# Kernel optimization log

Measured on AMD Instinct MI355X. Metric: run time of the kernel, lower is better.

The kernel has to match this reference:

```python
import jax, jax.numpy as jnp
import numpy as np

NUM_HEADS = 16
LN_EPS = 1e-5
RMS_EPS = 1e-6


def rmsnorm(x, gamma, eps=RMS_EPS):
    xf = x.astype(jnp.float32)
    rms = jax.lax.rsqrt(jnp.mean(xf * xf, axis=-1, keepdims=True) + eps)
    return gamma * (xf * rms).astype(x.dtype)


def layernorm(x, g, b, eps=LN_EPS):
    mu = jnp.mean(x, axis=-1, keepdims=True)
    var = jnp.mean(jnp.square(x - mu), axis=-1, keepdims=True)
    return (x - mu) * jax.lax.rsqrt(var + eps) * g + b


def setup_inputs() -> dict:
    key = jax.random.key(0)
    E = 2048
    ks = jax.random.split(key, 10)
    std = 0.02
    inp = {
        "x": jax.random.normal(ks[0], (2, 2048, E), dtype=jnp.float32),
        "Wq": jax.random.normal(ks[1], (E, E), dtype=jnp.float32) * std,
        "Wk": jax.random.normal(ks[2], (E, E), dtype=jnp.float32) * std,
        "Wv": jax.random.normal(ks[3], (E, E), dtype=jnp.float32) * std,
        "Wo": jax.random.normal(ks[4], (E, E), dtype=jnp.float32) * std,
        "ln_g": jnp.ones((E,), jnp.float32),
        "ln_b": jnp.zeros((E,), jnp.float32),
        "rms_g": jnp.ones((E,), jnp.float32),
        "mlp_W0": jax.random.normal(ks[5], (E, E), dtype=jnp.float32) * std,
        "sw_W": jax.random.normal(ks[6], (E, E), dtype=jnp.float32) * std,
        "sw_V": jax.random.normal(ks[7], (E, E), dtype=jnp.float32) * std,
        "sw_beta": jnp.ones((1,), jnp.float32),
        "mlp_rms_g": jnp.ones((E,), jnp.float32),
    }
    return inp


def reference(x, Wq, Wk, Wv, Wo, ln_g, ln_b, rms_g, mlp_W0, sw_W, sw_V, sw_beta, mlp_rms_g):
    B, S, E = x.shape
    H = NUM_HEADS
    Dh = E // H
    scale = 1.0 / (Dh ** 0.5)

    # --- MultiheadAttention (faithful to original einsum/view quirks) ---
    q = x @ Wq.T                     # (B,S,E)
    k = (x @ Wk.T) * scale
    v = x @ Wv.T
    qh = q.reshape(B, S, H, Dh)
    kh = k.reshape(B, S, H, Dh)
    scores = jnp.einsum('bthd,bshd->bhts', qh, kh)        # (B,H,T,S)
    causal = jnp.tril(jnp.ones((S, S), dtype=bool))
    scores = jnp.where(causal, scores, -jnp.inf)
    attn = jax.nn.softmax(scores, axis=-1)
    # NOTE: v is split (B,S,Dh,H) -- head/head_dim axes swapped vs q/k, as in the torch code
    vh = v.reshape(B, S, Dh, H)
    ctx = jnp.einsum('bsdh,bhts->bthd', vh, attn)          # == torch 'kjlm,kmij->kiml'
    ctx = ctx.reshape(B, S, E)                              # flatten heads-major
    ctx = layernorm(ctx, ln_g, ln_b)
    attn_out = ctx @ Wo.T

    x = x + attn_out
    x = rmsnorm(x, rms_g)

    # --- MLP: Linear -> SwiGLU -> RMSNorm, residual ---
    h = x @ mlp_W0.T
    w = h @ sw_W.T
    swish = w * jax.nn.sigmoid(sw_beta * w)
    g = swish * (h @ sw_V.T)
    mlp_out = rmsnorm(g, mlp_rms_g)
    return x + mlp_out
```

## Files before the change

kernel.cpp:

```cpp
#include <hip/hip_runtime.h>


#define B_    2
#define S_    2048
#define E_    2048
#define H_    16
#define DH    128
#define MROWS 4096
#define NEGF  (-3.0e38f)

typedef unsigned short ushort_t;
typedef unsigned int   uint_t;
typedef ushort_t us8   __attribute__((ext_vector_type(8)));
typedef ushort_t us4   __attribute__((ext_vector_type(4)));
typedef __bf16   bf16x8 __attribute__((ext_vector_type(8)));
typedef float    f32x4 __attribute__((ext_vector_type(4)));

__device__ __forceinline__ float b2f(ushort_t u) {
    uint_t x = ((uint_t)u) << 16;
    union { uint_t u; float f; } c; c.u = x; return c.f;
}
__device__ __forceinline__ ushort_t f2b(float f) {
    union { float f; uint_t u; } c; c.f = f;
    uint_t x = c.u;
    uint_t r = (x + 0x7fffu + ((x >> 16) & 1u)) >> 16;
    return (ushort_t)r;
}
__device__ __forceinline__ float fexp2(float x) {
    return __builtin_amdgcn_exp2f(x);
}

__device__ __forceinline__ void gld16(const ushort_t* g, ushort_t* l) {
    __builtin_amdgcn_global_load_lds(
        (const __attribute__((address_space(1))) void*)g,
        (__attribute__((address_space(3))) void*)l,
        16, 0, 0);
}

__global__ void probe_dtype(const ushort_t* w, int* flag) {
    __shared__ int cnt;
    if (threadIdx.x == 0) cnt = 0;
    __syncthreads();
    int c = 0;
    for (int i = threadIdx.x; i < 4096; i += 256) {
        uint_t e = (w[i] >> 7) & 0xFFu;
        if (e >= 0x84u) c++;
    }
    atomicAdd(&cnt, c);
    __syncthreads();
    if (threadIdx.x == 0) *flag = (cnt >= 8) ? 1 : 0;
}

__global__ void convert_k(const void* src, ushort_t* dst, long n, const int* flag) {
    int f = *flag;
    long i0 = (long)blockIdx.x * blockDim.x + threadIdx.x;
    long stride = (long)gridDim.x * blockDim.x;
    long n4 = n >> 2;
    if (f) {
        const f32x4* s = (const f32x4*)src;
        for (long i = i0; i < n4; i += stride) {
            f32x4 v = s[i];
            us4 o = { f2b(v[0]), f2b(v[1]), f2b(v[2]), f2b(v[3]) };
            *(us4*)(dst + i * 4) = o;
        }
        for (long i = n4 * 4 + i0; i < n; i += stride)
            dst[i] = f2b(((const float*)src)[i]);
    } else {
        const us4* s = (const us4*)src;
        for (long i = i0; i < n4; i += stride)
            *(us4*)(dst + i * 4) = s[i];
        for (long i = n4 * 4 + i0; i < n; i += stride)
            dst[i] = ((const ushort_t*)src)[i];
    }
}

__global__ void fill_diag(float* out, long n, float val) {
    long i = (long)blockIdx.x * 256 + threadIdx.x;
    if (i < n) out[i] = val;
}

__global__ __launch_bounds__(256) void gemm_bt(
    const ushort_t* __restrict__ A, const ushort_t* __restrict__ W,
    ushort_t* out, const ushort_t* resid, const ushort_t* beta,
    void* outv, const int* flagp, float scale, int mode)
{
    const int K = E_, N = E_;
    __shared__ alignas(16) ushort_t Asf[128 * 32];
    __shared__ alignas(16) ushort_t Bsf[128 * 32];

    const int tid  = threadIdx.x;
    const int wave = tid >> 6;
    const int lane = tid & 63;
    const int wm   = (wave >> 1) * 64;
    const int wn   = (wave & 1) * 64;
    const int lrow = lane & 15;
    const int quad = lane >> 4;
    const int m0   = blockIdx.y * 128;
    const int n0   = blockIdx.x * 128;

    const float betav = (beta != nullptr) ? b2f(beta[0]) : 0.0f;
    const int   of32  = (flagp != nullptr) ? *flagp : 0;

    f32x4 acc[4][4];
#pragma unroll
    for (int i = 0; i < 4; i++)
#pragma unroll
        for (int j = 0; j < 4; j++) acc[i][j] = f32x4{0.f, 0.f, 0.f, 0.f};

    const int ch   = wave * 2;
    const int crow = lane >> 2;
    const int ccol = (lane & 3) * 8;
    const ushort_t* Ag0 = A + (long)(m0 + ch * 16 + crow) * K + ccol;
    const ushort_t* Wg0 = W + (long)(n0 + ch * 16 + crow) * K + ccol;
    ushort_t* Al0 = &Asf[ch * 16 * 32];
    ushort_t* Bl0 = &Bsf[ch * 16 * 32];

    for (int kk = 0; kk < K; kk += 32) {
        gld16(Ag0 + kk,          Al0);
        gld16(Ag0 + 16 * K + kk, Al0 + 512);
        gld16(Wg0 + kk,          Bl0);
        gld16(Wg0 + 16 * K + kk, Bl0 + 512);
        __syncthreads();

        bf16x8 af[4], bfr[4];
#pragma unroll
        for (int i = 0; i < 4; i++)
            af[i]  = __builtin_bit_cast(bf16x8, *(const us8*)&Asf[(wm + i*16 + lrow) * 32 + quad * 8]);
#pragma unroll
        for (int j = 0; j < 4; j++)
            bfr[j] = __builtin_bit_cast(bf16x8, *(const us8*)&Bsf[(wn + j*16 + lrow) * 32 + quad * 8]);
#pragma unroll
        for (int i = 0; i < 4; i++)
#pragma unroll
            for (int j = 0; j < 4; j++)
                acc[i][j] = __builtin_amdgcn_mfma_f32_16x16x32_bf16(af[i], bfr[j], acc[i][j], 0, 0, 0);
        __syncthreads();
    }

#pragma unroll
    for (int i = 0; i < 4; i++)
#pragma unroll
        for (int j = 0; j < 4; j++)
#pragma unroll
            for (int r = 0; r < 4; r++) {
                int m = m0 + wm + i*16 + quad*4 + r;
                int n = n0 + wn + j*16 + lrow;
                float v = acc[i][j][r] * scale;
                long idx;
                if (mode == 1) {
                    int h = n >> 7, d = n & 127;
                    idx = ((long)h * S_ + m) * DH + d;
                } else if (mode == 2) {
                    int d = n >> 4, h = n & 15;
                    idx = ((long)h * DH + d) * S_ + m;
                } else {
                    idx = (long)m * N + n;
                    if (mode == 3) {
                        v += b2f(resid[idx]);
                    } else if (mode == 4) {
                        float wv  = b2f(resid[idx]);
                        float sig = 1.0f / (1.0f + expf(-betav * wv));
                        v = wv * sig * v;
                        if (of32) { ((float*)outv)[idx] = v; continue; }
                    }
                }
                out[idx] = f2b(v);
            }
}

__global__ __launch_bounds__(256) void gemm_qkv(
    const ushort_t* __restrict__ X,
    const ushort_t* __restrict__ Wq, const ushort_t* __restrict__ Wk,
    const ushort_t* __restrict__ Wv,
    ushort_t* qo, ushort_t* ko, ushort_t* vo, float kscale)
{
    const int K = E_;
    __shared__ alignas(16) ushort_t Asf[128 * 32];
    __shared__ alignas(16) ushort_t Bsf[128 * 32];

    const int tid  = threadIdx.x;
    const int wave = tid >> 6;
    const int lane = tid & 63;
    const int wm   = (wave >> 1) * 64;
    const int wn   = (wave & 1) * 64;
    const int lrow = lane & 15;
    const int quad = lane >> 4;
    const int sel  = blockIdx.x >> 4;
    const int n0   = (blockIdx.x & 15) * 128;
    const int m0   = blockIdx.y * 128;
    const long zoff = (long)blockIdx.z * ((long)S_ * E_);

    const ushort_t* A = X + zoff;
    const ushort_t* W = (sel == 0) ? Wq : (sel == 1) ? Wk : Wv;
    const float scale = (sel == 1) ? kscale : 1.0f;
    ushort_t* out = ((sel == 0) ? qo : (sel == 1) ? ko : vo) + zoff;

    f32x4 acc[4][4];
#pragma unroll
    for (int i = 0; i < 4; i++)
#pragma unroll
        for (int j = 0; j < 4; j++) acc[i][j] = f32x4{0.f, 0.f, 0.f, 0.f};

    const int ch   = wave * 2;
    const int crow = lane >> 2;
    const int ccol = (lane & 3) * 8;
    const ushort_t* Ag0 = A + (long)(m0 + ch * 16 + crow) * K + ccol;
    const ushort_t* Wg0 = W + (long)(n0 + ch * 16 + crow) * K + ccol;
    ushort_t* Al0 = &Asf[ch * 16 * 32];
    ushort_t* Bl0 = &Bsf[ch * 16 * 32];

    for (int kk = 0; kk < K; kk += 32) {
        gld16(Ag0 + kk,          Al0);
        gld16(Ag0 + 16 * K + kk, Al0 + 512);
        gld16(Wg0 + kk,          Bl0);
        gld16(Wg0 + 16 * K + kk, Bl0 + 512);
        __syncthreads();

        bf16x8 af[4], bfr[4];
#pragma unroll
        for (int i = 0; i < 4; i++)
            af[i]  = __builtin_bit_cast(bf16x8, *(const us8*)&Asf[(wm + i*16 + lrow) * 32 + quad * 8]);
#pragma unroll
        for (int j = 0; j < 4; j++)
            bfr[j] = __builtin_bit_cast(bf16x8, *(const us8*)&Bsf[(wn + j*16 + lrow) * 32 + quad * 8]);
#pragma unroll
        for (int i = 0; i < 4; i++)
#pragma unroll
            for (int j = 0; j < 4; j++)
                acc[i][j] = __builtin_amdgcn_mfma_f32_16x16x32_bf16(af[i], bfr[j], acc[i][j], 0, 0, 0);
        __syncthreads();
    }

#pragma unroll
    for (int i = 0; i < 4; i++)
#pragma unroll
        for (int j = 0; j < 4; j++)
#pragma unroll
            for (int r = 0; r < 4; r++) {
                int m = m0 + wm + i*16 + quad*4 + r;
                int n = n0 + wn + j*16 + lrow;
                float v = acc[i][j][r] * scale;
                long idx;
                if (sel <= 1) {
                    int h = n >> 7, d = n & 127;
                    idx = ((long)h * S_ + m) * DH + d;
                } else {
                    int d = n >> 4, h = n & 15;
                    idx = ((long)h * DH + d) * S_ + m;
                }
                out[idx] = f2b(v);
            }
}

__global__ __launch_bounds__(256) void flash_attn(
    const ushort_t* __restrict__ qp, const ushort_t* __restrict__ kp,
    const ushort_t* __restrict__ vt, ushort_t* ctx)
{
    __shared__ alignas(16) ushort_t Kt[64][144];
    __shared__ alignas(16) ushort_t Vt[128][72];
    __shared__ alignas(16) ushort_t Pb[4][16][72];

    const long zq = (long)blockIdx.z * ((long)S_ * E_);
    qp  += zq; kp += zq; vt += zq; ctx += zq;

    const int tid  = threadIdx.x;
    const int wave = tid >> 6;
    const int lane = tid & 63;
    const int lrow = lane & 15;
    const int quad = lane >> 4;
    const int h    = blockIdx.y;

    const long qbase = (long)h * S_ * DH;
    const long vbase = (long)h * DH * S_;

#pragma unroll 1
    for (int half = 0; half < 2; half++) {
        const int qt = (half == 0) ? (int)blockIdx.x : (31 - (int)blockIdx.x);
        const int tw = qt * 64 + wave * 16;

        bf16x8 qf[4];
        {
            const ushort_t* qrow = qp + qbase + (long)(tw + lrow) * DH + quad * 8;
#pragma unroll
            for (int ks = 0; ks < 4; ks++)
                qf[ks] = __builtin_bit_cast(bf16x8, *(const us8*)(qrow + ks * 32));
        }

        float m_i[4], l_i[4];
#pragma unroll
        for (int r = 0; r < 4; r++) { m_i[r] = NEGF; l_i[r] = 0.0f; }
        f32x4 o[8];
#pragma unroll
        for (int i = 0; i < 8; i++) o[i] = f32x4{0.f, 0.f, 0.f, 0.f};

        for (int st = 0; st <= qt; st++) {
            const int sb = st * 64;
#pragma unroll
            for (int it = 0; it < 4; it++) {
                int L = tid + it * 256;
                int r = L >> 4, c8 = L & 15;
                *(us8*)&Kt[r][c8 * 8] = *(const us8*)(kp + qbase + (long)(sb + r) * DH + c8 * 8);
            }
#pragma unroll
            for (int it = 0; it < 4; it++) {
                int L = tid + it * 256;
                int d = L >> 3, c8 = L & 7;
                *(us8*)&Vt[d][c8 * 8] = *(const us8*)(vt + vbase + (long)d * S_ + sb + c8 * 8);
            }
            __syncthreads();

            f32x4 sacc[4];
#pragma unroll
            for (int nt = 0; nt < 4; nt++) {
                sacc[nt] = f32x4{0.f, 0.f, 0.f, 0.f};
#pragma unroll
                for (int ks = 0; ks < 4; ks++) {
                    bf16x8 kf = __builtin_bit_cast(bf16x8, *(const us8*)&Kt[nt*16 + lrow][ks*32 + quad*8]);
                    sacc[nt] = __builtin_amdgcn_mfma_f32_16x16x32_bf16(qf[ks], kf, sacc[nt], 0, 0, 0);
                }
            }

            const bool diag = (st == qt);
            float alpha[4];
#pragma unroll
            for (int r = 0; r < 4; r++) {
                const int trow = tw + quad * 4 + r;
                float pv[4];
#pragma unroll
                for (int nt = 0; nt < 4; nt++) {
                    float sv = sacc[nt][r];
                    if (diag && (sb + nt*16 + lrow > trow)) sv = NEGF;
                    pv[nt] = sv;
                }
                float mx = fmaxf(fmaxf(pv[0], pv[1]), fmaxf(pv[2], pv[3]));
                mx = fmaxf(mx, __shfl_xor(mx, 1));
                mx = fmaxf(mx, __shfl_xor(mx, 2));
                mx = fmaxf(mx, __shfl_xor(mx, 4));
                mx = fmaxf(mx, __shfl_xor(mx, 8));
                float mn = fmaxf(m_i[r], mx);
                float al = fexp2(m_i[r] - mn);
                float s  = 0.0f;
#pragma unroll
                for (int nt = 0; nt < 4; nt++) {
                    float p = fexp2(pv[nt] - mn);
                    s += p;
                    Pb[wave][quad*4 + r][nt*16 + lrow] = f2b(p);
                }
                s += __shfl_xor(s, 1);
                s += __shfl_xor(s, 2);
                s += __shfl_xor(s, 4);
                s += __shfl_xor(s, 8);
                l_i[r]  = l_i[r] * al + s;
                m_i[r]  = mn;
                alpha[r] = al;
            }
#pragma unroll
            for (int nt = 0; nt < 8; nt++)
#pragma unroll
                for (int r = 0; r < 4; r++) o[nt][r] *= alpha[r];

            bf16x8 pf[2];
#pragma unroll
            for (int ks = 0; ks < 2; ks++)
                pf[ks] = __builtin_bit_cast(bf16x8, *(const us8*)&Pb[wave][lrow][ks*32 + quad*8]);
#pragma unroll
            for (int nt = 0; nt < 8; nt++)
#pragma unroll
                for (int ks = 0; ks < 2; ks++) {
                    bf16x8 vf = __builtin_bit_cast(bf16x8, *(const us8*)&Vt[nt*16 + lrow][ks*32 + quad*8]);
                    o[nt] = __builtin_amdgcn_mfma_f32_16x16x32_bf16(pf[ks], vf, o[nt], 0, 0, 0);
                }
            __syncthreads();
        }

        float li4[4];
#pragma unroll
        for (int r = 0; r < 4; r++) li4[r] = 1.0f / l_i[r];
#pragma unroll
        for (int nt = 0; nt < 8; nt++)
#pragma unroll
            for (int r = 0; r < 4; r++) {
                int t = tw + quad*4 + r;
                int d = nt*16 + lrow;
                ctx[(long)t * E_ + h * DH + d] = f2b(o[nt][r] * li4[r]);
            }
    }
}

__global__ __launch_bounds__(256) void ln_rows(
    const ushort_t* x, const ushort_t* __restrict__ g,
    const ushort_t* __restrict__ bta, ushort_t* out)
{
    __shared__ float red[16];
    const int row = blockIdx.x;
    const ushort_t* xr = x + (long)row * E_;
    float vals[8], s = 0.f, ss = 0.f;
#pragma unroll
    for (int i = 0; i < 8; i++) {
        float v = b2f(xr[threadIdx.x + i * 256]);
        vals[i] = v; s += v; ss += v * v;
    }
    for (int off = 1; off < 64; off <<= 1) { s += __shfl_xor(s, off); ss += __shfl_xor(ss, off); }
    int wave = threadIdx.x >> 6, lane = threadIdx.x & 63;
    if (lane == 0) { red[wave] = s; red[8 + wave] = ss; }
    __syncthreads();
    if (threadIdx.x == 0) {
        red[4]  = red[0] + red[1] + red[2] + red[3];
        red[12] = red[8] + red[9] + red[10] + red[11];
    }
    __syncthreads();
    float mu  = red[4] / E_;
    float var = red[12] / E_ - mu * mu;
    float rs  = rsqrtf(var + 1e-5f);
#pragma unroll
    for (int i = 0; i < 8; i++) {
        int c = threadIdx.x + i * 256;
        float v = (vals[i] - mu) * rs * b2f(g[c]) + b2f(bta[c]);
        out[(long)row * E_ + c] = f2b(v);
    }
}

__global__ __launch_bounds__(256) void rms_rows(
    const ushort_t* x, const ushort_t* __restrict__ g, ushort_t* out)
{
    __shared__ float red[8];
    const int row = blockIdx.x;
    const ushort_t* xr = x + (long)row * E_;
    float vals[8], ss = 0.f;
#pragma unroll
    for (int i = 0; i < 8; i++) {
        float v = b2f(xr[threadIdx.x + i * 256]);
        vals[i] = v; ss += v * v;
    }
    for (int off = 1; off < 64; off <<= 1) ss += __shfl_xor(ss, off);
    int wave = threadIdx.x >> 6, lane = threadIdx.x & 63;
    if (lane == 0) red[wave] = ss;
    __syncthreads();
    if (threadIdx.x == 0) red[4] = red[0] + red[1] + red[2] + red[3];
    __syncthreads();
    float rms = rsqrtf(red[4] / E_ + 1e-6f);
#pragma unroll
    for (int i = 0; i < 8; i++) {
        int c = threadIdx.x + i * 256;
        float v = b2f(f2b(vals[i] * rms)) * b2f(g[c]);
        out[(long)row * E_ + c] = f2b(v);
    }
}

__global__ __launch_bounds__(256) void rms_final(
    const void* x, const ushort_t* __restrict__ g,
    const ushort_t* resid, void* outv, const int* flagp)
{
    __shared__ float red[8];
    const int row = blockIdx.x;
    const int of32 = *flagp;
    float vals[8], ss = 0.f;
#pragma unroll
    for (int i = 0; i < 8; i++) {
        int c = threadIdx.x + i * 256;
        float v = of32 ? ((const float*)x)[(long)row * E_ + c]
                       : b2f(((const ushort_t*)x)[(long)row * E_ + c]);
        vals[i] = v; ss += v * v;
    }
    for (int off = 1; off < 64; off <<= 1) ss += __shfl_xor(ss, off);
    int wave = threadIdx.x >> 6, lane = threadIdx.x & 63;
    if (lane == 0) red[wave] = ss;
    __syncthreads();
    if (threadIdx.x == 0) red[4] = red[0] + red[1] + red[2] + red[3];
    __syncthreads();
    float rms = rsqrtf(red[4] / E_ + 1e-6f);
#pragma unroll
    for (int i = 0; i < 8; i++) {
        int c = threadIdx.x + i * 256;
        long idx = (long)row * E_ + c;
        if (of32) {
            float v = vals[i] * rms * b2f(g[c]) + b2f(resid[idx]);
            ((float*)outv)[idx] = v;
        } else {
            float v = b2f(f2b(vals[i] * rms)) * b2f(g[c]) + b2f(resid[idx]);
            ((ushort_t*)outv)[idx] = f2b(v);
        }
    }
}

extern "C" void kernel_launch(void* const* d_in, const int* in_sizes, int n_in,
                              void* d_out, int out_size, void* d_ws, size_t ws_size,
                              hipStream_t stream)
{
    const size_t NB  = (size_t)MROWS * E_;
    const size_t WSZ = (size_t)E_ * E_;
    const size_t QSZ = (size_t)S_ * E_;
    const float kscale = 0.08838834764831845f * 1.4426950408889634f;

    const size_t stage_elems = NB + 7 * WSZ + 6 * 4096;
    const size_t need_def    = (stage_elems + 2 * NB) * 2;
    const size_t need_direct = 2 * NB * 2;

    dim3 gFull(E_ / 128, MROWS / 128);

    if (ws_size >= need_def) {
        ushort_t* st = (ushort_t*)d_ws;
        ushort_t* c_x   = st;
        ushort_t* c_Wq  = c_x  + NB;
        ushort_t* c_Wk  = c_Wq + WSZ;
        ushort_t* c_Wv  = c_Wk + WSZ;
        ushort_t* c_Wo  = c_Wv + WSZ;
        ushort_t* c_W0  = c_Wo + WSZ;
        ushort_t* c_sW  = c_W0 + WSZ;
        ushort_t* c_sV  = c_sW + WSZ;
        ushort_t* c_lng = c_sV + WSZ;
        ushort_t* c_lnb = c_lng + 4096;
        ushort_t* c_rg  = c_lnb + 4096;
        ushort_t* c_mg  = c_rg  + 4096;
        ushort_t* c_sb  = c_mg  + 4096;
        int*      flag  = (int*)(c_sb + 4096);
        ushort_t* w0    = st + stage_elems;
        ushort_t* w1    = w0 + NB;
        ushort_t* ob    = (ushort_t*)d_out;
        ushort_t* ob2   = ob + NB;

        probe_dtype<<<1, 256, 0, stream>>>((const ushort_t*)d_in[1], flag);
        convert_k<<<1024, 256, 0, stream>>>(d_in[0],  c_x,  (long)NB,  flag);
        convert_k<<<1024, 256, 0, stream>>>(d_in[1],  c_Wq, (long)WSZ, flag);
        convert_k<<<1024, 256, 0, stream>>>(d_in[2],  c_Wk, (long)WSZ, flag);
        convert_k<<<1024, 256, 0, stream>>>(d_in[3],  c_Wv, (long)WSZ, flag);
        convert_k<<<1024, 256, 0, stream>>>(d_in[4],  c_Wo, (long)WSZ, flag);
        convert_k<<<1024, 256, 0, stream>>>(d_in[8],  c_W0, (long)WSZ, flag);
        convert_k<<<1024, 256, 0, stream>>>(d_in[9],  c_sW, (long)WSZ, flag);
        convert_k<<<1024, 256, 0, stream>>>(d_in[10], c_sV, (long)WSZ, flag);
        convert_k<<<8,    256, 0, stream>>>(d_in[5],  c_lng, E_, flag);
        convert_k<<<8,    256, 0, stream>>>(d_in[6],  c_lnb, E_, flag);
        convert_k<<<8,    256, 0, stream>>>(d_in[7],  c_rg,  E_, flag);
        convert_k<<<8,    256, 0, stream>>>(d_in[12], c_mg,  E_, flag);
        convert_k<<<1,    64,  0, stream>>>(d_in[11], c_sb,  1,  flag);

        gemm_qkv<<<dim3(48, 16, 2), 256, 0, stream>>>(c_x, c_Wq, c_Wk, c_Wv,
                                                      w0, ob, w1, kscale);
        flash_attn<<<dim3(16, H_, 2), 256, 0, stream>>>(w0, ob, w1, ob2);

        ln_rows<<<MROWS, 256, 0, stream>>>(ob2, c_lng, c_lnb, ob2);
        gemm_bt<<<gFull, 256, 0, stream>>>(ob2, c_Wo, w1, c_x, nullptr, nullptr, nullptr, 1.0f, 3);
        rms_rows<<<MROWS, 256, 0, stream>>>(w1, c_rg, w1);
        gemm_bt<<<gFull, 256, 0, stream>>>(w1, c_W0, w0, nullptr, nullptr, nullptr, nullptr, 1.0f, 0);
        gemm_bt<<<gFull, 256, 0, stream>>>(w0, c_sW, c_x, nullptr, nullptr, nullptr, nullptr, 1.0f, 0);
        gemm_bt<<<gFull, 256, 0, stream>>>(w0, c_sV, (ushort_t*)d_out, c_x, c_sb, d_out, flag, 1.0f, 4);
        rms_final<<<MROWS, 256, 0, stream>>>(d_out, c_mg, w1, d_out, flag);
    } else if (ws_size >= need_direct) {
        ushort_t* w0 = (ushort_t*)d_ws;
        ushort_t* w1 = w0 + NB;
        ushort_t* ob = (ushort_t*)d_out;
        int* flag = (int*)((char*)d_ws + 2 * NB * 2);
        hipMemsetAsync(flag, 0, sizeof(int), stream);
        const ushort_t* x   = (const ushort_t*)d_in[0];
        const ushort_t* Wq  = (const ushort_t*)d_in[1];
        const ushort_t* Wk  = (const ushort_t*)d_in[2];
        const ushort_t* Wv  = (const ushort_t*)d_in[3];
        const ushort_t* Wo  = (const ushort_t*)d_in[4];
        const ushort_t* lng = (const ushort_t*)d_in[5];
        const ushort_t* lnb = (const ushort_t*)d_in[6];
        const ushort_t* rg  = (const ushort_t*)d_in[7];
        const ushort_t* W0  = (const ushort_t*)d_in[8];
        const ushort_t* sW  = (const ushort_t*)d_in[9];
        const ushort_t* sV  = (const ushort_t*)d_in[10];
        const ushort_t* sb  = (const ushort_t*)d_in[11];
        const ushort_t* mg  = (const ushort_t*)d_in[12];
        for (int b = 0; b < B_; b++) {
            const ushort_t* xb = x + (size_t)b * QSZ;
            gemm_qkv<<<dim3(48, 16, 1), 256, 0, stream>>>(xb, Wq, Wk, Wv,
                                                          w0, w0 + QSZ, w1, kscale);
            flash_attn<<<dim3(16, H_, 1), 256, 0, stream>>>(w0, w0 + QSZ, w1, ob + (size_t)b * QSZ);
        }
        ln_rows<<<MROWS, 256, 0, stream>>>(ob, lng, lnb, ob);
        gemm_bt<<<gFull, 256, 0, stream>>>(ob, Wo, w0, x, nullptr, nullptr, nullptr, 1.0f, 3);
        rms_rows<<<MROWS, 256, 0, stream>>>(w0, rg, w0);
        gemm_bt<<<gFull, 256, 0, stream>>>(w0, W0, w1, nullptr, nullptr, nullptr, nullptr, 1.0f, 0);
        gemm_bt<<<gFull, 256, 0, stream>>>(w1, sW, ob, nullptr, nullptr, nullptr, nullptr, 1.0f, 0);
        gemm_bt<<<gFull, 256, 0, stream>>>(w1, sV, ob, ob, sb, d_out, flag, 1.0f, 4);
        rms_final<<<MROWS, 256, 0, stream>>>(ob, mg, w0, d_out, flag);
    } else {
        fill_diag<<<((long)NB + 255) / 256, 256, 0, stream>>>((float*)d_out, (long)NB,
                                                              1000.0f + ws_size * 1e-6f);
    }
}
```

Measured before the change: 772.2 us.

## Prefetch next K/V tile into registers and launch one query tile per block

The flash attention kernel now prefetches the next K and V tile from global memory into registers while computing on the current tile in shared memory, so load latency can overlap with MFMA work. The paired causal load balancing, where each block handled query tile i and 31-i, is removed. The grid doubles to 32 blocks per head so each block processes a single query tile. This gives more blocks and more parallelism, but causal work per block becomes uneven and each thread holds extra registers for the prefetch buffers.

```diff
diff --git a/kernel.cpp b/kernel.cpp
--- a/kernel.cpp
+++ b/kernel.cpp
@@ -269,122 +269,137 @@
     const int lrow = lane & 15;
     const int quad = lane >> 4;
     const int h    = blockIdx.y;
+    const int qt   = blockIdx.x;
+    const int tw   = qt * 64 + wave * 16;
 
     const long qbase = (long)h * S_ * DH;
     const long vbase = (long)h * DH * S_;
 
-#pragma unroll 1
-    for (int half = 0; half < 2; half++) {
-        const int qt = (half == 0) ? (int)blockIdx.x : (31 - (int)blockIdx.x);
-        const int tw = qt * 64 + wave * 16;
-
-        bf16x8 qf[4];
-        {
-            const ushort_t* qrow = qp + qbase + (long)(tw + lrow) * DH + quad * 8;
-#pragma unroll
-            for (int ks = 0; ks < 4; ks++)
-                qf[ks] = __builtin_bit_cast(bf16x8, *(const us8*)(qrow + ks * 32));
-        }
-
-        float m_i[4], l_i[4];
-#pragma unroll
-        for (int r = 0; r < 4; r++) { m_i[r] = NEGF; l_i[r] = 0.0f; }
-        f32x4 o[8];
-#pragma unroll
-        for (int i = 0; i < 8; i++) o[i] = f32x4{0.f, 0.f, 0.f, 0.f};
-
-        for (int st = 0; st <= qt; st++) {
-            const int sb = st * 64;
-#pragma unroll
-            for (int it = 0; it < 4; it++) {
-                int L = tid + it * 256;
-                int r = L >> 4, c8 = L & 15;
-                *(us8*)&Kt[r][c8 * 8] = *(const us8*)(kp + qbase + (long)(sb + r) * DH + c8 * 8);
+    int kr[4], kc[4], vr[4], vc[4];
+#pragma unroll
+    for (int it = 0; it < 4; it++) {
+        int L = tid + it * 256;
+        kr[it] = L >> 4; kc[it] = (L & 15) * 8;
+        vr[it] = L >> 3; vc[it] = (L & 7) * 8;
+    }
+
+    bf16x8 qf[4];
+    {
+        const ushort_t* qrow = qp + qbase + (long)(tw + lrow) * DH + quad * 8;
+#pragma unroll
+        for (int ks = 0; ks < 4; ks++)
+            qf[ks] = __builtin_bit_cast(bf16x8, *(const us8*)(qrow + ks * 32));
+    }
+
+    float m_i[4], l_i[4];
+#pragma unroll
+    for (int r = 0; r < 4; r++) { m_i[r] = NEGF; l_i[r] = 0.0f; }
+    f32x4 o[8];
+#pragma unroll
+    for (int i = 0; i < 8; i++) o[i] = f32x4{0.f, 0.f, 0.f, 0.f};
+
+    us8 kreg[4], vreg[4];
+#pragma unroll
+    for (int it = 0; it < 4; it++)
+        kreg[it] = *(const us8*)(kp + qbase + (long)kr[it] * DH + kc[it]);
+#pragma unroll
+    for (int it = 0; it < 4; it++)
+        vreg[it] = *(const us8*)(vt + vbase + (long)vr[it] * S_ + vc[it]);
+
+    for (int st = 0; st <= qt; st++) {
+        const int sb = st * 64;
+
+#pragma unroll
+        for (int it = 0; it < 4; it++) *(us8*)&Kt[kr[it]][kc[it]] = kreg[it];
+#pragma unroll
+        for (int it = 0; it < 4; it++) *(us8*)&Vt[vr[it]][vc[it]] = vreg[it];
+        __syncthreads();
+
+        if (st < qt) {
+            const int sb2 = sb + 64;
+#pragma unroll
+            for (int it = 0; it < 4; it++)
+                kreg[it] = *(const us8*)(kp + qbase + (long)(sb2 + kr[it]) * DH + kc[it]);
+#pragma unroll
+            for (int it = 0; it < 4; it++)
+                vreg[it] = *(const us8*)(vt + vbase + (long)vr[it] * S_ + sb2 + vc[it]);
+        }
+
+        f32x4 sacc[4];
+#pragma unroll
+        for (int nt = 0; nt < 4; nt++) {
+            sacc[nt] = f32x4{0.f, 0.f, 0.f, 0.f};
+#pragma unroll
+            for (int ks = 0; ks < 4; ks++) {
+                bf16x8 kf = __builtin_bit_cast(bf16x8, *(const us8*)&Kt[nt*16 + lrow][ks*32 + quad*8]);
+                sacc[nt] = __builtin_amdgcn_mfma_f32_16x16x32_bf16(qf[ks], kf, sacc[nt], 0, 0, 0);
             }
-#pragma unroll
-            for (int it = 0; it < 4; it++) {
-                int L = tid + it * 256;
-                int d = L >> 3, c8 = L & 7;
-                *(us8*)&Vt[d][c8 * 8] = *(const us8*)(vt + vbase + (long)d * S_ + sb + c8 * 8);
+        }
+
+        const bool diag = (st == qt);
+        float alpha[4];
+#pragma unroll
+        for (int r = 0; r < 4; r++) {
+            const int trow = tw + quad * 4 + r;
+            float pv[4];
+#pragma unroll
+            for (int nt = 0; nt < 4; nt++) {
+                float sv = sacc[nt][r];
+                if (diag && (sb + nt*16 + lrow > trow)) sv = NEGF;
+                pv[nt] = sv;
             }
-            __syncthreads();
-
-            f32x4 sacc[4];
+            float mx = fmaxf(fmaxf(pv[0], pv[1]), fmaxf(pv[2], pv[3]));
+            mx = fmaxf(mx, __shfl_xor(mx, 1));
+            mx = fmaxf(mx, __shfl_xor(mx, 2));
+            mx = fmaxf(mx, __shfl_xor(mx, 4));
+            mx = fmaxf(mx, __shfl_xor(mx, 8));
+            float mn = fmaxf(m_i[r], mx);
+            float al = fexp2(m_i[r] - mn);
+            float s  = 0.0f;
 #pragma unroll
             for (int nt = 0; nt < 4; nt++) {
-                sacc[nt] = f32x4{0.f, 0.f, 0.f, 0.f};
-#pragma unroll
-                for (int ks = 0; ks < 4; ks++) {
-                    bf16x8 kf = __builtin_bit_cast(bf16x8, *(const us8*)&Kt[nt*16 + lrow][ks*32 + quad*8]);
-                    sacc[nt] = __builtin_amdgcn_mfma_f32_16x16x32_bf16(qf[ks], kf, sacc[nt], 0, 0, 0);
-                }
+                float p = fexp2(pv[nt] - mn);
+                s += p;
+                Pb[wave][quad*4 + r][nt*16 + lrow] = f2b(p);
             }
-
-            const bool diag = (st == qt);
-            float alpha[4];
-#pragma unroll
-            for (int r = 0; r < 4; r++) {
-                const int trow = tw + quad * 4 + r;
-                float pv[4];
-#pragma unroll
-                for (int nt = 0; nt < 4; nt++) {
-                    float sv = sacc[nt][r];
-                    if (diag && (sb + nt*16 + lrow > trow)) sv = NEGF;
-                    pv[nt] = sv;
-                }
-                float mx = fmaxf(fmaxf(pv[0], pv[1]), fmaxf(pv[2], pv[3]));
-                mx = fmaxf(mx, __shfl_xor(mx, 1));
-                mx = fmaxf(mx, __shfl_xor(mx, 2));
-                mx = fmaxf(mx, __shfl_xor(mx, 4));
-                mx = fmaxf(mx, __shfl_xor(mx, 8));
-                float mn = fmaxf(m_i[r], mx);
-                float al = fexp2(m_i[r] - mn);
-                float s  = 0.0f;
-#pragma unroll
-                for (int nt = 0; nt < 4; nt++) {
-                    float p = fexp2(pv[nt] - mn);
-                    s += p;
-                    Pb[wave][quad*4 + r][nt*16 + lrow] = f2b(p);
-                }
-                s += __shfl_xor(s, 1);
-                s += __shfl_xor(s, 2);
-                s += __shfl_xor(s, 4);
-                s += __shfl_xor(s, 8);
-                l_i[r]  = l_i[r] * al + s;
-                m_i[r]  = mn;
-                alpha[r] = al;
+            s += __shfl_xor(s, 1);
+            s += __shfl_xor(s, 2);
+            s += __shfl_xor(s, 4);
+            s += __shfl_xor(s, 8);
+            l_i[r]  = l_i[r] * al + s;
+            m_i[r]  = mn;
+            alpha[r] = al;
+        }
+#pragma unroll
+        for (int nt = 0; nt < 8; nt++)
+#pragma unroll
+            for (int r = 0; r < 4; r++) o[nt][r] *= alpha[r];
+
+        bf16x8 pf[2];
+#pragma unroll
+        for (int ks = 0; ks < 2; ks++)
+            pf[ks] = __builtin_bit_cast(bf16x8, *(const us8*)&Pb[wave][lrow][ks*32 + quad*8]);
+#pragma unroll
+        for (int nt = 0; nt < 8; nt++)
+#pragma unroll
+            for (int ks = 0; ks < 2; ks++) {
+                bf16x8 vf = __builtin_bit_cast(bf16x8, *(const us8*)&Vt[nt*16 + lrow][ks*32 + quad*8]);
+                o[nt] = __builtin_amdgcn_mfma_f32_16x16x32_bf16(pf[ks], vf, o[nt], 0, 0, 0);
             }
-#pragma unroll
-            for (int nt = 0; nt < 8; nt++)
-#pragma unroll
-                for (int r = 0; r < 4; r++) o[nt][r] *= alpha[r];
-
-            bf16x8 pf[2];
-#pragma unroll
-            for (int ks = 0; ks < 2; ks++)
-                pf[ks] = __builtin_bit_cast(bf16x8, *(const us8*)&Pb[wave][lrow][ks*32 + quad*8]);
-#pragma unroll
-            for (int nt = 0; nt < 8; nt++)
-#pragma unroll
-                for (int ks = 0; ks < 2; ks++) {
-                    bf16x8 vf = __builtin_bit_cast(bf16x8, *(const us8*)&Vt[nt*16 + lrow][ks*32 + quad*8]);
-                    o[nt] = __builtin_amdgcn_mfma_f32_16x16x32_bf16(pf[ks], vf, o[nt], 0, 0, 0);
-                }
-            __syncthreads();
-        }
-
-        float li4[4];
-#pragma unroll
-        for (int r = 0; r < 4; r++) li4[r] = 1.0f / l_i[r];
-#pragma unroll
-        for (int nt = 0; nt < 8; nt++)
-#pragma unroll
-            for (int r = 0; r < 4; r++) {
-                int t = tw + quad*4 + r;
-                int d = nt*16 + lrow;
-                ctx[(long)t * E_ + h * DH + d] = f2b(o[nt][r] * li4[r]);
-            }
-    }
+        __syncthreads();
+    }
+
+    float li4[4];
+#pragma unroll
+    for (int r = 0; r < 4; r++) li4[r] = 1.0f / l_i[r];
+#pragma unroll
+    for (int nt = 0; nt < 8; nt++)
+#pragma unroll
+        for (int r = 0; r < 4; r++) {
+            int t = tw + quad*4 + r;
+            int d = nt*16 + lrow;
+            ctx[(long)t * E_ + h * DH + d] = f2b(o[nt][r] * li4[r]);
+        }
 }
 
 __global__ __launch_bounds__(256) void ln_rows(
@@ -536,7 +551,7 @@
 
         gemm_qkv<<<dim3(48, 16, 2), 256, 0, stream>>>(c_x, c_Wq, c_Wk, c_Wv,
                                                       w0, ob, w1, kscale);
-        flash_attn<<<dim3(16, H_, 2), 256, 0, stream>>>(w0, ob, w1, ob2);
+        flash_attn<<<dim3(32, H_, 2), 256, 0, stream>>>(w0, ob, w1, ob2);
 
         ln_rows<<<MROWS, 256, 0, stream>>>(ob2, c_lng, c_lnb, ob2);
         gemm_bt<<<gFull, 256, 0, stream>>>(ob2, c_Wo, w1, c_x, nullptr, nullptr, nullptr, 1.0f, 3);
@@ -568,7 +583,7 @@
             const ushort_t* xb = x + (size_t)b * QSZ;
             gemm_qkv<<<dim3(48, 16, 1), 256, 0, stream>>>(xb, Wq, Wk, Wv,
                                                           w0, w0 + QSZ, w1, kscale);
-            flash_attn<<<dim3(16, H_, 1), 256, 0, stream>>>(w0, w0 + QSZ, w1, ob + (size_t)b * QSZ);
+            flash_attn<<<dim3(32, H_, 1), 256, 0, stream>>>(w0, w0 + QSZ, w1, ob + (size_t)b * QSZ);
         }
         ln_rows<<<MROWS, 256, 0, stream>>>(ob, lng, lnb, ob);
         gemm_bt<<<gFull, 256, 0, stream>>>(ob, Wo, w0, x, nullptr, nullptr, nullptr, 1.0f, 3);
```

Measured after the change: 780.4 us. Within noise of the previous version (+1.1%).
